# Kernel tuning notes

Hardware: AMD Instinct MI355X
Metric: run time of the kernel (lower is better)

Reference implementation:

```python
import jax, jax.numpy as jnp
import numpy as np

COMMIT_LAMBDA = 0.25


def setup_inputs() -> dict:
    key = jax.random.key(0)
    k1, k2 = jax.random.split(key)
    B, C, T = 8, 256, 1024
    NCB, K, D = 2, 8192, 128
    x = jax.random.normal(k1, (B, C, T), dtype=jnp.float32)
    # EMA codebook weights buffer (init: randn * 0.1)
    codebooks = jax.random.normal(k2, (NCB, K, D), dtype=jnp.float32) * 0.1
    return {"x": x, "codebooks": codebooks}


def reference(x, codebooks):
    B, C, T = x.shape
    ncb, K, d = codebooks.shape
    # [B, C, T] -> [B*T, ncb, d]
    xs = x.reshape(B, ncb, d, T).transpose(0, 3, 1, 2).reshape(B * T, ncb, d)
    # squared euclidean distances (argmin-equivalent to cdist)
    x2 = jnp.sum(xs * xs, axis=-1)[..., None]            # [N, ncb, 1]
    c2 = jnp.sum(codebooks * codebooks, axis=-1)[None]    # [1, ncb, K]
    xc = jnp.einsum('bnd,nkd->bnk', xs, codebooks)        # [N, ncb, K]
    d2 = x2 - 2.0 * xc + c2
    idx = jnp.argmin(d2, axis=-1)                         # [N, ncb] int
    # gather nearest code vectors: [N, ncb, d]
    q = codebooks[jnp.arange(ncb)[None, :], idx]
    # straight-through estimator
    q_st = xs + jax.lax.stop_gradient(q - xs)
    # commitment loss (training mode): sum over codebooks of mse(x_i, q_i.detach())
    loss = COMMIT_LAMBDA * jnp.sum(
        jnp.mean((xs - jax.lax.stop_gradient(q)) ** 2, axis=(0, 2))
    )
    # reassemble to [B, C, T]
    quantized = q_st.reshape(B, T, ncb, d).transpose(0, 2, 3, 1).reshape(B, C, T)
    indices = idx.reshape(B, T, ncb).transpose(0, 2, 1)   # [B, ncb, T]
    return quantized, indices, loss
```

## Files before the change

### kernel.cpp

```cpp
#include <hip/hip_runtime.h>
#include <hip/hip_bf16.h>

#define BB   8
#define TT   1024
#define NCBN 2
#define DD   128
#define KK   8192
#define MM   8192

constexpr int OUT_IDX_OFF  = BB * 256 * TT;
constexpr int OUT_LOSS_OFF = OUT_IDX_OFF + BB * NCBN * TT;

#define THR   0.45f
#define QCAP  2048
#define SCAP  2048

typedef __attribute__((ext_vector_type(8))) short   short8;
typedef __attribute__((ext_vector_type(4))) float   float4v;

__device__ __forceinline__ unsigned short f2bf(float v) {
    unsigned u = __float_as_uint(v);
    return (unsigned short)((u + 0x7FFFu + ((u >> 16) & 1u)) >> 16);
}

__device__ __forceinline__ unsigned short f2bf_dn(float v) {
    unsigned u = __float_as_uint(v);
    unsigned short h = (unsigned short)(u >> 16);
    if ((u & 0x80000000u) && (u & 0xFFFFu)) ++h;
    return h;
}

__device__ __forceinline__ void gl_lds16(const void* g, void* l) {
    __builtin_amdgcn_global_load_lds(
        (const __attribute__((address_space(1))) unsigned int*)g,
        (__attribute__((address_space(3))) unsigned int*)l, 16, 0, 0);
}

__global__ __launch_bounds__(256)
void pack_kernel(const float* __restrict__ x, const float* __restrict__ cb,
                 unsigned short* __restrict__ xbf, unsigned short* __restrict__ cbf,
                 float* __restrict__ x2, float* __restrict__ c2,
                 unsigned long long* __restrict__ pmin, float* __restrict__ out) {
    __shared__ float Ld[DD][33];
    const int gb  = blockIdx.x;
    const int tid = threadIdx.x;

    if (gb < 512) {
        const int bxn = gb & 15, ty = gb >> 4;
        const int b = bxn >> 1, n = bxn & 1;
        const int t0 = ty * 32;

        const float* base = x + ((size_t)(b * 256 + n * 128)) * TT + t0;
#pragma unroll
        for (int pp = 0; pp < 4; ++pp) {
            int u = tid + pp * 256;
            int d = u >> 3, sg = u & 7;
            float4 v = *(const float4*)(base + (size_t)d * TT + sg * 4);
            int t = sg * 4;
            Ld[d][t + 0] = v.x; Ld[d][t + 1] = v.y;
            Ld[d][t + 2] = v.z; Ld[d][t + 3] = v.w;
        }
        __syncthreads();

        if (tid < 32) {
            float s = 0.f;
            for (int d = 0; d < DD; ++d) { float v = Ld[d][tid]; s = fmaf(v, v, s); }
            x2[(size_t)n * MM + b * TT + t0 + tid] = s;
            pmin[(size_t)n * MM + b * TT + t0 + tid] = 0xFFFFFFFFFFFFFFFFull;
        }

        unsigned short* orow0 = xbf + ((size_t)n * MM + b * TT + t0) * DD;
#pragma unroll
        for (int pp = 0; pp < 2; ++pp) {
            int u = tid + pp * 256;
            int tt = u >> 4, sg = u & 15;
            unsigned short tmp[8];
#pragma unroll
            for (int j = 0; j < 8; ++j) tmp[j] = f2bf(Ld[sg * 8 + j][tt]);
            uint4 pk;
            pk.x = (unsigned)tmp[0] | ((unsigned)tmp[1] << 16);
            pk.y = (unsigned)tmp[2] | ((unsigned)tmp[3] << 16);
            pk.z = (unsigned)tmp[4] | ((unsigned)tmp[5] << 16);
            pk.w = (unsigned)tmp[6] | ((unsigned)tmp[7] << 16);
            *(uint4*)(orow0 + (size_t)tt * DD + sg * 8) = pk;
        }
    } else {
        int g = (gb - 512) * 256 + tid;
        if (g == 0) out[OUT_LOSS_OFF] = 0.f;
        const float4* crow = (const float4*)(cb + (size_t)g * DD);
        unsigned short* orow = cbf + (size_t)g * DD;
        float s = 0.f;
#pragma unroll 4
        for (int i2 = 0; i2 < 16; ++i2) {
            float4 v0 = crow[2 * i2];
            float4 v1 = crow[2 * i2 + 1];
            s = fmaf(v0.x, v0.x, s); s = fmaf(v0.y, v0.y, s);
            s = fmaf(v0.z, v0.z, s); s = fmaf(v0.w, v0.w, s);
            s = fmaf(v1.x, v1.x, s); s = fmaf(v1.y, v1.y, s);
            s = fmaf(v1.z, v1.z, s); s = fmaf(v1.w, v1.w, s);
            uint4 pk;
            pk.x = (unsigned)f2bf(v0.x) | ((unsigned)f2bf(v0.y) << 16);
            pk.y = (unsigned)f2bf(v0.z) | ((unsigned)f2bf(v0.w) << 16);
            pk.z = (unsigned)f2bf(v1.x) | ((unsigned)f2bf(v1.y) << 16);
            pk.w = (unsigned)f2bf(v1.z) | ((unsigned)f2bf(v1.w) << 16);
            *(uint4*)(orow + i2 * 8) = pk;
        }
        c2[g] = s;
    }
}

__device__ void rescore_one(int n, int m, int k,
                            const float* __restrict__ x, const float* __restrict__ cb,
                            const float* __restrict__ x2, const float* __restrict__ c2,
                            unsigned long long* __restrict__ pmin) {
    int b = m >> 10, t = m & (TT - 1);
    const float* xp = x + ((size_t)(b * 256 + n * 128)) * TT + t;
    const float* cp = cb + ((size_t)(n * KK + k)) * DD;
    float xc = 0.f;
    for (int d = 0; d < DD; ++d)
        xc = fmaf(xp[(size_t)d * TT], cp[d], xc);
    float u = x2[n * MM + m] - 2.0f * xc;
    float s = u + c2[n * KK + k];
    unsigned long long pk = ((unsigned long long)__float_as_uint(s) << 32) | (unsigned)k;
    atomicMin(pmin + (size_t)n * MM + m, pk);
}

__global__ __launch_bounds__(512, 4)
void screen_kernel(const unsigned short* __restrict__ xbf,
                   const unsigned short* __restrict__ cbf,
                   const float* __restrict__ c2,
                   const float* __restrict__ x,
                   const float* __restrict__ cb32,
                   const float* __restrict__ x2,
                   unsigned long long* __restrict__ pmin,
                   unsigned long long* __restrict__ spill) {
    __shared__ __align__(16) unsigned short Csh[2][128 * 128];
    __shared__ float          c2s[2][128];
    __shared__ unsigned int   minU[128];
    __shared__ unsigned int   qcnt;
    __shared__ unsigned int   queue[QCAP];
    __shared__ unsigned short queueY[QCAP];

    const int tid = threadIdx.x;
    const int id  = blockIdx.x;
    const int n   = id & 1;
    const int ks  = (id >> 1) & 3;
    const int qt  = id >> 3;
    const int m0  = qt * 128;
    const int k0  = ks * 2048;

    const int wave = tid >> 6, lane = tid & 63;
    const int cw = wave & 1, qw = wave >> 1;
    const int quad = lane >> 4, l15 = lane & 15;

    unsigned long long* spillp = spill + (size_t)id * SCAP;

    int goff[4];
#pragma unroll
    for (int p = 0; p < 4; ++p) {
        int u   = (p * 8 + wave) * 64 + lane;
        int row = u >> 4;
        int seg = (u & 15) ^ (row & 15);
        goff[p] = (row * DD + seg * 8) * 2;
    }

    const char*  asrc0 = (const char*)(cbf + ((size_t)n * KK + k0) * DD);
    const float* c2p   = c2 + (size_t)n * KK + k0;

    {
        const char* qsrc = (const char*)(xbf + ((size_t)n * MM + m0) * DD);
#pragma unroll
        for (int p = 0; p < 4; ++p)
            gl_lds16(qsrc + goff[p], &Csh[0][(p * 8 + wave) * 512]);
#pragma unroll
        for (int p = 0; p < 4; ++p)
            gl_lds16(asrc0 + goff[p], &Csh[1][(p * 8 + wave) * 512]);
    }
    if (tid < 32)  *(float4*)&c2s[1][tid * 4] = *(const float4*)(c2p + tid * 4);
    if (tid < 128) minU[tid] = 0xFFFFFFFFu;
    if (tid == 0)  qcnt = 0;
    __syncthreads();

    short8 bfr[2][4];
#pragma unroll
    for (int tq = 0; tq < 2; ++tq) {
        int q = qw * 32 + tq * 16 + l15;
#pragma unroll
        for (int k4 = 0; k4 < 4; ++k4) {
            int seg = k4 * 4 + quad;
            bfr[tq][k4] = *(const short8*)(&Csh[0][q * 128 + ((seg ^ l15) * 8)]);
        }
    }
    __syncthreads();

    float thr[2] = {3.4e38f, 3.4e38f};

    for (int it = 0; it <= 16; ++it) {
        const int sb   = it & 1;
        const int cbuf = sb ^ 1;
        const int dcur = (it < 16) ? it : 0;

        if (it < 16) {
            const int dn = (it + 1 < 16) ? (it + 1) : 0;
            const char* src = asrc0 + (size_t)dn * (128 * DD * 2);
#pragma unroll
            for (int p = 0; p < 4; ++p)
                gl_lds16(src + goff[p], &Csh[sb][(p * 8 + wave) * 512]);
            if (tid < 32)
                *(float4*)&c2s[sb][tid * 4] =
                    *(const float4*)(c2p + dn * 128 + tid * 4);
        }

        float4v acc[4][2];
#pragma unroll
        for (int tc = 0; tc < 4; ++tc)
#pragma unroll
            for (int tq = 0; tq < 2; ++tq)
                acc[tc][tq] = (float4v){0.f, 0.f, 0.f, 0.f};

#pragma unroll
        for (int k4 = 0; k4 < 4; ++k4) {
            short8 a[4];
#pragma unroll
            for (int tc = 0; tc < 4; ++tc) {
                int r = cw * 64 + tc * 16 + l15;
                int seg = k4 * 4 + quad;
                a[tc] = *(const short8*)(&Csh[cbuf][r * 128 + ((seg ^ l15) * 8)]);
            }
#pragma unroll
            for (int tc = 0; tc < 4; ++tc)
#pragma unroll
                for (int tq = 0; tq < 2; ++tq)
                    acc[tc][tq] = __builtin_amdgcn_mfma_f32_16x16x32_bf16(
                        a[tc], bfr[tq][k4], acc[tc][tq], 0, 0, 0);
        }

        float cmin[2] = {3.4e38f, 3.4e38f};
#pragma unroll
        for (int tc = 0; tc < 4; ++tc) {
            float4v c2r = *(const float4v*)(&c2s[cbuf][cw * 64 + tc * 16 + quad * 4]);
#pragma unroll
            for (int tq = 0; tq < 2; ++tq) {
                float y0 = fmaf(-2.0f, acc[tc][tq][0], c2r[0]);
                float y1 = fmaf(-2.0f, acc[tc][tq][1], c2r[1]);
                float y2 = fmaf(-2.0f, acc[tc][tq][2], c2r[2]);
                float y3 = fmaf(-2.0f, acc[tc][tq][3], c2r[3]);
                acc[tc][tq] = (float4v){y0, y1, y2, y3};
                cmin[tq] = fminf(cmin[tq],
                                 fminf(fminf(y0, y1), fminf(y2, y3)));
            }
        }
#pragma unroll
        for (int tq = 0; tq < 2; ++tq) {
            float v = cmin[tq];
            v = fminf(v, __shfl_xor(v, 16, 64));
            v = fminf(v, __shfl_xor(v, 32, 64));
            cmin[tq] = v;
        }

        if (it > 0) {
            float te[2];
#pragma unroll
            for (int tq = 0; tq < 2; ++tq)
                te[tq] = fminf(thr[tq], cmin[tq] + THR);
#pragma unroll
            for (int tc = 0; tc < 4; ++tc) {
#pragma unroll
                for (int tq = 0; tq < 2; ++tq) {
                    float4v yv = acc[tc][tq];
                    float m4 = fminf(fminf(yv[0], yv[1]), fminf(yv[2], yv[3]));
                    if (m4 <= te[tq]) {
#pragma unroll
                        for (int rg = 0; rg < 4; ++rg) {
                            if (yv[rg] <= te[tq]) {
                                unsigned idx  = atomicAdd(&qcnt, 1u);
                                unsigned code = (unsigned)(dcur * 128 + cw * 64 + tc * 16 + quad * 4 + rg);
                                unsigned q    = (unsigned)(qw * 32 + tq * 16 + l15);
                                unsigned ent  = (q << 11) | code;
                                if (idx < QCAP) {
                                    queue[idx]  = ent;
                                    queueY[idx] = f2bf_dn(yv[rg]);
                                } else if (idx < QCAP + SCAP) {
                                    spillp[idx - QCAP] =
                                        ((unsigned long long)ent << 32) |
                                        (unsigned long long)f2bf_dn(yv[rg]);
                                } else {
                                    rescore_one(n, m0 + (int)q, k0 + (int)code,
                                                x, cb32, x2, c2, pmin);
                                }
                            }
                        }
                    }
                }
            }
        }

        if (it < 16) {
#pragma unroll
            for (int tq = 0; tq < 2; ++tq) {
                if (quad == 0) {
                    unsigned u  = __float_as_uint(cmin[tq]);
                    unsigned mu = (u & 0x80000000u) ? ~u : (u | 0x80000000u);
                    atomicMin(&minU[qw * 32 + tq * 16 + l15], mu);
                }
            }
        }
        __syncthreads();
        if (it < 16) {
#pragma unroll
            for (int tq = 0; tq < 2; ++tq) {
                unsigned mu = minU[qw * 32 + tq * 16 + l15];
                unsigned u  = (mu & 0x80000000u) ? (mu & 0x7FFFFFFFu) : ~mu;
                thr[tq] = __uint_as_float(u) + THR;
            }
        }
    }

    unsigned total = qcnt;
    if (total > (unsigned)(QCAP + SCAP)) total = QCAP + SCAP;
    for (unsigned i = tid; i < total; i += 512) {
        unsigned ent; unsigned short y16;
        if (i < QCAP) { ent = queue[i]; y16 = queueY[i]; }
        else {
            unsigned long long se = spillp[i - QCAP];
            ent = (unsigned)(se >> 32); y16 = (unsigned short)se;
        }
        unsigned q   = ent >> 11;
        unsigned mu  = minU[q];
        unsigned u   = (mu & 0x80000000u) ? (mu & 0x7FFFFFFFu) : ~mu;
        float thrF   = __uint_as_float(u) + THR;
        float yv     = __uint_as_float((unsigned)y16 << 16);
        if (yv <= thrF)
            rescore_one(n, m0 + (int)q, k0 + (int)(ent & 2047u),
                        x, cb32, x2, c2, pmin);
    }
}

__global__ __launch_bounds__(256)
void gather_kernel(const float* __restrict__ cb,
                   const unsigned long long* __restrict__ pmin,
                   float* __restrict__ out) {
    __shared__ float Cr[32][DD + 1];
    __shared__ int   kid[32];
    const int b = blockIdx.x >> 1, n = blockIdx.x & 1;
    const int t0 = blockIdx.y * 32;
    const int tid = threadIdx.x;

    float spart = 0.f;
    if (tid < 32) {
        int t = t0 + tid;
        unsigned long long pk = pmin[(size_t)n * MM + b * TT + t];
        int k = (int)(pk & 0xFFFFFFFFull);
        kid[tid] = k;
        out[OUT_IDX_OFF + (b * NCBN + n) * TT + t] = (float)k;
        spart = __uint_as_float((unsigned)(pk >> 32));
    }
    __syncthreads();

    {
        int row = tid >> 3, q8 = tid & 7;
        const float* cp = cb + ((size_t)n * KK + kid[row]) * DD + q8 * 16;
#pragma unroll
        for (int j = 0; j < 4; ++j) {
            float4 v = *(const float4*)(cp + j * 4);
            int d = q8 * 16 + j * 4;
            Cr[row][d + 0] = v.x; Cr[row][d + 1] = v.y;
            Cr[row][d + 2] = v.z; Cr[row][d + 3] = v.w;
        }
    }
    __syncthreads();

    float* ob = out + ((size_t)(b * 256 + n * 128)) * TT + t0;
#pragma unroll
    for (int pp = 0; pp < 4; ++pp) {
        int u  = tid + pp * 256;
        int d  = u >> 3, ts = (u & 7) * 4;
        float4 qv = { Cr[ts + 0][d], Cr[ts + 1][d], Cr[ts + 2][d], Cr[ts + 3][d] };
        *(float4*)(ob + (size_t)d * TT + ts) = qv;
    }

    if (tid < 32) {
#pragma unroll
        for (int o = 16; o > 0; o >>= 1) spart += __shfl_down(spart, o, 64);
        if (tid == 0)
            atomicAdd(out + OUT_LOSS_OFF, spart * 2.384185791015625e-7f);
    }
}

extern "C" void kernel_launch(void* const* d_in, const int* in_sizes, int n_in,
                              void* d_out, int out_size, void* d_ws, size_t ws_size,
                              hipStream_t stream) {
    (void)in_sizes; (void)n_in; (void)out_size; (void)ws_size;
    const float* x  = (const float*)d_in[0];
    const float* cb = (const float*)d_in[1];
    float* out = (float*)d_out;

    char* ws = (char*)d_ws;
    unsigned short* xbf = (unsigned short*)(ws);
    unsigned short* cbf = (unsigned short*)(ws + (4u << 20));
    float* x2 = (float*)(ws + (8u << 20));
    float* c2 = (float*)(ws + (8u << 20) + (64u << 10));
    unsigned long long* pmin =
        (unsigned long long*)(ws + (8u << 20) + (128u << 10));

    unsigned long long* spill = (unsigned long long*)out;

    pack_kernel<<<dim3(576), 256, 0, stream>>>(x, cb, xbf, cbf, x2, c2, pmin, out);
    screen_kernel<<<dim3(512), 512, 0, stream>>>(xbf, cbf, c2, x, cb, x2, pmin,
                                                 spill);
    gather_kernel<<<dim3(16, 32), 256, 0, stream>>>(cb, pmin, out);
}
```

Baseline: 183.3 us.

## Filter candidates in the same iteration, dropping the extra pipeline stage

Removes the delayed-by-one-iteration candidate filtering and the 17th loop iteration. Each tile is now filtered right after its MFMA pass, using the shared running minimum read directly from LDS. The c2 values are loaded before a barrier that is moved earlier, so the buffer can be overwritten safely. The minU sentinel is changed to the encoding of the max float so the threshold stays finite. Because minU is read without a barrier after other waves update it, the threshold can be looser, which may enqueue more candidates.

```diff
diff --git a/kernel.cpp b/kernel.cpp
--- a/kernel.cpp
+++ b/kernel.cpp
@@ -177,7 +177,7 @@
             gl_lds16(asrc0 + goff[p], &Csh[1][(p * 8 + wave) * 512]);
     }
     if (tid < 32)  *(float4*)&c2s[1][tid * 4] = *(const float4*)(c2p + tid * 4);
-    if (tid < 128) minU[tid] = 0xFFFFFFFFu;
+    if (tid < 128) minU[tid] = 0xFF7FFFFFu;
     if (tid == 0)  qcnt = 0;
     __syncthreads();
 
@@ -193,15 +193,12 @@
     }
     __syncthreads();
 
-    float thr[2] = {3.4e38f, 3.4e38f};
-
-    for (int it = 0; it <= 16; ++it) {
+    for (int it = 0; it < 16; ++it) {
         const int sb   = it & 1;
         const int cbuf = sb ^ 1;
-        const int dcur = (it < 16) ? it : 0;
-
-        if (it < 16) {
-            const int dn = (it + 1 < 16) ? (it + 1) : 0;
+
+        if (it < 15) {
+            const int dn = it + 1;
             const char* src = asrc0 + (size_t)dn * (128 * DD * 2);
 #pragma unroll
             for (int p = 0; p < 4; ++p)
@@ -235,19 +232,27 @@
                         a[tc], bfr[tq][k4], acc[tc][tq], 0, 0, 0);
         }
 
+        float4v c2r[4];
+#pragma unroll
+        for (int tc = 0; tc < 4; ++tc)
+            c2r[tc] = *(const float4v*)(&c2s[cbuf][cw * 64 + tc * 16 + quad * 4]);
+
+        __syncthreads();
+
         float cmin[2] = {3.4e38f, 3.4e38f};
+        float m4s[4][2];
 #pragma unroll
         for (int tc = 0; tc < 4; ++tc) {
-            float4v c2r = *(const float4v*)(&c2s[cbuf][cw * 64 + tc * 16 + quad * 4]);
 #pragma unroll
             for (int tq = 0; tq < 2; ++tq) {
-                float y0 = fmaf(-2.0f, acc[tc][tq][0], c2r[0]);
-                float y1 = fmaf(-2.0f, acc[tc][tq][1], c2r[1]);
-                float y2 = fmaf(-2.0f, acc[tc][tq][2], c2r[2]);
-                float y3 = fmaf(-2.0f, acc[tc][tq][3], c2r[3]);
+                float y0 = fmaf(-2.0f, acc[tc][tq][0], c2r[tc][0]);
+                float y1 = fmaf(-2.0f, acc[tc][tq][1], c2r[tc][1]);
+                float y2 = fmaf(-2.0f, acc[tc][tq][2], c2r[tc][2]);
+                float y3 = fmaf(-2.0f, acc[tc][tq][3], c2r[tc][3]);
                 acc[tc][tq] = (float4v){y0, y1, y2, y3};
-                cmin[tq] = fminf(cmin[tq],
-                                 fminf(fminf(y0, y1), fminf(y2, y3)));
+                float m4 = fminf(fminf(y0, y1), fminf(y2, y3));
+                m4s[tc][tq] = m4;
+                cmin[tq] = fminf(cmin[tq], m4);
             }
         }
 #pragma unroll
@@ -258,36 +263,37 @@
             cmin[tq] = v;
         }
 
-        if (it > 0) {
-            float te[2];
-#pragma unroll
-            for (int tq = 0; tq < 2; ++tq)
-                te[tq] = fminf(thr[tq], cmin[tq] + THR);
-#pragma unroll
-            for (int tc = 0; tc < 4; ++tc) {
-#pragma unroll
-                for (int tq = 0; tq < 2; ++tq) {
+        float te[2];
+#pragma unroll
+        for (int tq = 0; tq < 2; ++tq) {
+            unsigned mu = minU[qw * 32 + tq * 16 + l15];
+            unsigned u  = (mu & 0x80000000u) ? (mu & 0x7FFFFFFFu) : ~mu;
+            te[tq] = fminf(__uint_as_float(u) + THR, cmin[tq] + THR);
+        }
+
+#pragma unroll
+        for (int tc = 0; tc < 4; ++tc) {
+#pragma unroll
+            for (int tq = 0; tq < 2; ++tq) {
+                if (m4s[tc][tq] <= te[tq]) {
                     float4v yv = acc[tc][tq];
-                    float m4 = fminf(fminf(yv[0], yv[1]), fminf(yv[2], yv[3]));
-                    if (m4 <= te[tq]) {
-#pragma unroll
-                        for (int rg = 0; rg < 4; ++rg) {
-                            if (yv[rg] <= te[tq]) {
-                                unsigned idx  = atomicAdd(&qcnt, 1u);
-                                unsigned code = (unsigned)(dcur * 128 + cw * 64 + tc * 16 + quad * 4 + rg);
-                                unsigned q    = (unsigned)(qw * 32 + tq * 16 + l15);
-                                unsigned ent  = (q << 11) | code;
-                                if (idx < QCAP) {
-                                    queue[idx]  = ent;
-                                    queueY[idx] = f2bf_dn(yv[rg]);
-                                } else if (idx < QCAP + SCAP) {
-                                    spillp[idx - QCAP] =
-                                        ((unsigned long long)ent << 32) |
-                                        (unsigned long long)f2bf_dn(yv[rg]);
-                                } else {
-                                    rescore_one(n, m0 + (int)q, k0 + (int)code,
-                                                x, cb32, x2, c2, pmin);
-                                }
+#pragma unroll
+                    for (int rg = 0; rg < 4; ++rg) {
+                        if (yv[rg] <= te[tq]) {
+                            unsigned idx  = atomicAdd(&qcnt, 1u);
+                            unsigned code = (unsigned)(it * 128 + cw * 64 + tc * 16 + quad * 4 + rg);
+                            unsigned q    = (unsigned)(qw * 32 + tq * 16 + l15);
+                            unsigned ent  = (q << 11) | code;
+                            if (idx < QCAP) {
+                                queue[idx]  = ent;
+                                queueY[idx] = f2bf_dn(yv[rg]);
+                            } else if (idx < QCAP + SCAP) {
+                                spillp[idx - QCAP] =
+                                    ((unsigned long long)ent << 32) |
+                                    (unsigned long long)f2bf_dn(yv[rg]);
+                            } else {
+                                rescore_one(n, m0 + (int)q, k0 + (int)code,
+                                            x, cb32, x2, c2, pmin);
                             }
                         }
                     }
@@ -295,26 +301,17 @@
             }
         }
 
-        if (it < 16) {
-#pragma unroll
-            for (int tq = 0; tq < 2; ++tq) {
-                if (quad == 0) {
-                    unsigned u  = __float_as_uint(cmin[tq]);
-                    unsigned mu = (u & 0x80000000u) ? ~u : (u | 0x80000000u);
-                    atomicMin(&minU[qw * 32 + tq * 16 + l15], mu);
-                }
+#pragma unroll
+        for (int tq = 0; tq < 2; ++tq) {
+            if (quad == 0) {
+                unsigned u  = __float_as_uint(cmin[tq]);
+                unsigned mu = (u & 0x80000000u) ? ~u : (u | 0x80000000u);
+                atomicMin(&minU[qw * 32 + tq * 16 + l15], mu);
             }
         }
-        __syncthreads();
-        if (it < 16) {
-#pragma unroll
-            for (int tq = 0; tq < 2; ++tq) {
-                unsigned mu = minU[qw * 32 + tq * 16 + l15];
-                unsigned u  = (mu & 0x80000000u) ? (mu & 0x7FFFFFFFu) : ~mu;
-                thr[tq] = __uint_as_float(u) + THR;
-            }
-        }
-    }
+    }
+
+    __syncthreads();
 
     unsigned total = qcnt;
     if (total > (unsigned)(QCAP + SCAP)) total = QCAP + SCAP;
```

Measured after the change: 250.0 us. 36.4% more time.

## Double screen kernel block to 1024 threads, halving per-wave query tile

Applied to the files above, without the earlier changes.

The screening kernel now runs 16 waves per block instead of 8. Each wave handles 16 query rows instead of 32, so per-thread accumulators and B fragments are halved and the cooperative LDS loads use two passes instead of four. The goal is lower register pressure and more waves to hide LDS and MFMA latency. In exchange, each A fragment loaded from LDS now feeds only one MFMA instead of two, which doubles LDS read traffic per MFMA and may add barrier cost with more waves per block.

```diff
diff --git a/kernel.cpp b/kernel.cpp
--- a/kernel.cpp
+++ b/kernel.cpp
@@ -125,7 +125,7 @@
     atomicMin(pmin + (size_t)n * MM + m, pk);
 }
 
-__global__ __launch_bounds__(512, 4)
+__global__ __launch_bounds__(1024, 8)
 void screen_kernel(const unsigned short* __restrict__ xbf,
                    const unsigned short* __restrict__ cbf,
                    const float* __restrict__ c2,
@@ -155,10 +155,10 @@
 
     unsigned long long* spillp = spill + (size_t)id * SCAP;
 
-    int goff[4];
-#pragma unroll
-    for (int p = 0; p < 4; ++p) {
-        int u   = (p * 8 + wave) * 64 + lane;
+    int goff[2];
+#pragma unroll
+    for (int p = 0; p < 2; ++p) {
+        int u   = (p * 16 + wave) * 64 + lane;
         int row = u >> 4;
         int seg = (u & 15) ^ (row & 15);
         goff[p] = (row * DD + seg * 8) * 2;
@@ -170,30 +170,29 @@
     {
         const char* qsrc = (const char*)(xbf + ((size_t)n * MM + m0) * DD);
 #pragma unroll
-        for (int p = 0; p < 4; ++p)
-            gl_lds16(qsrc + goff[p], &Csh[0][(p * 8 + wave) * 512]);
-#pragma unroll
-        for (int p = 0; p < 4; ++p)
-            gl_lds16(asrc0 + goff[p], &Csh[1][(p * 8 + wave) * 512]);
+        for (int p = 0; p < 2; ++p)
+            gl_lds16(qsrc + goff[p], &Csh[0][(p * 16 + wave) * 512]);
+#pragma unroll
+        for (int p = 0; p < 2; ++p)
+            gl_lds16(asrc0 + goff[p], &Csh[1][(p * 16 + wave) * 512]);
     }
     if (tid < 32)  *(float4*)&c2s[1][tid * 4] = *(const float4*)(c2p + tid * 4);
     if (tid < 128) minU[tid] = 0xFFFFFFFFu;
     if (tid == 0)  qcnt = 0;
     __syncthreads();
 
-    short8 bfr[2][4];
-#pragma unroll
-    for (int tq = 0; tq < 2; ++tq) {
-        int q = qw * 32 + tq * 16 + l15;
+    short8 bfr[4];
+    {
+        int q = qw * 16 + l15;
 #pragma unroll
         for (int k4 = 0; k4 < 4; ++k4) {
             int seg = k4 * 4 + quad;
-            bfr[tq][k4] = *(const short8*)(&Csh[0][q * 128 + ((seg ^ l15) * 8)]);
+            bfr[k4] = *(const short8*)(&Csh[0][q * 128 + ((seg ^ l15) * 8)]);
         }
     }
     __syncthreads();
 
-    float thr[2] = {3.4e38f, 3.4e38f};
+    float thr = 3.4e38f;
 
     for (int it = 0; it <= 16; ++it) {
         const int sb   = it & 1;
@@ -204,19 +203,17 @@
             const int dn = (it + 1 < 16) ? (it + 1) : 0;
             const char* src = asrc0 + (size_t)dn * (128 * DD * 2);
 #pragma unroll
-            for (int p = 0; p < 4; ++p)
-                gl_lds16(src + goff[p], &Csh[sb][(p * 8 + wave) * 512]);
+            for (int p = 0; p < 2; ++p)
+                gl_lds16(src + goff[p], &Csh[sb][(p * 16 + wave) * 512]);
             if (tid < 32)
                 *(float4*)&c2s[sb][tid * 4] =
                     *(const float4*)(c2p + dn * 128 + tid * 4);
         }
 
-        float4v acc[4][2];
+        float4v acc[4];
 #pragma unroll
         for (int tc = 0; tc < 4; ++tc)
-#pragma unroll
-            for (int tq = 0; tq < 2; ++tq)
-                acc[tc][tq] = (float4v){0.f, 0.f, 0.f, 0.f};
+            acc[tc] = (float4v){0.f, 0.f, 0.f, 0.f};
 
 #pragma unroll
         for (int k4 = 0; k4 < 4; ++k4) {
@@ -229,65 +226,48 @@
             }
 #pragma unroll
             for (int tc = 0; tc < 4; ++tc)
-#pragma unroll
-                for (int tq = 0; tq < 2; ++tq)
-                    acc[tc][tq] = __builtin_amdgcn_mfma_f32_16x16x32_bf16(
-                        a[tc], bfr[tq][k4], acc[tc][tq], 0, 0, 0);
-        }
-
-        float cmin[2] = {3.4e38f, 3.4e38f};
+                acc[tc] = __builtin_amdgcn_mfma_f32_16x16x32_bf16(
+                    a[tc], bfr[k4], acc[tc], 0, 0, 0);
+        }
+
+        float cmin = 3.4e38f;
 #pragma unroll
         for (int tc = 0; tc < 4; ++tc) {
             float4v c2r = *(const float4v*)(&c2s[cbuf][cw * 64 + tc * 16 + quad * 4]);
-#pragma unroll
-            for (int tq = 0; tq < 2; ++tq) {
-                float y0 = fmaf(-2.0f, acc[tc][tq][0], c2r[0]);
-                float y1 = fmaf(-2.0f, acc[tc][tq][1], c2r[1]);
-                float y2 = fmaf(-2.0f, acc[tc][tq][2], c2r[2]);
-                float y3 = fmaf(-2.0f, acc[tc][tq][3], c2r[3]);
-                acc[tc][tq] = (float4v){y0, y1, y2, y3};
-                cmin[tq] = fminf(cmin[tq],
-                                 fminf(fminf(y0, y1), fminf(y2, y3)));
-            }
-        }
-#pragma unroll
-        for (int tq = 0; tq < 2; ++tq) {
-            float v = cmin[tq];
-            v = fminf(v, __shfl_xor(v, 16, 64));
-            v = fminf(v, __shfl_xor(v, 32, 64));
-            cmin[tq] = v;
-        }
+            float y0 = fmaf(-2.0f, acc[tc][0], c2r[0]);
+            float y1 = fmaf(-2.0f, acc[tc][1], c2r[1]);
+            float y2 = fmaf(-2.0f, acc[tc][2], c2r[2]);
+            float y3 = fmaf(-2.0f, acc[tc][3], c2r[3]);
+            acc[tc] = (float4v){y0, y1, y2, y3};
+            cmin = fminf(cmin, fminf(fminf(y0, y1), fminf(y2, y3)));
+        }
+        cmin = fminf(cmin, __shfl_xor(cmin, 16, 64));
+        cmin = fminf(cmin, __shfl_xor(cmin, 32, 64));
 
         if (it > 0) {
-            float te[2];
-#pragma unroll
-            for (int tq = 0; tq < 2; ++tq)
-                te[tq] = fminf(thr[tq], cmin[tq] + THR);
+            float te = fminf(thr, cmin + THR);
 #pragma unroll
             for (int tc = 0; tc < 4; ++tc) {
-#pragma unroll
-                for (int tq = 0; tq < 2; ++tq) {
-                    float4v yv = acc[tc][tq];
-                    float m4 = fminf(fminf(yv[0], yv[1]), fminf(yv[2], yv[3]));
-                    if (m4 <= te[tq]) {
-#pragma unroll
-                        for (int rg = 0; rg < 4; ++rg) {
-                            if (yv[rg] <= te[tq]) {
-                                unsigned idx  = atomicAdd(&qcnt, 1u);
-                                unsigned code = (unsigned)(dcur * 128 + cw * 64 + tc * 16 + quad * 4 + rg);
-                                unsigned q    = (unsigned)(qw * 32 + tq * 16 + l15);
-                                unsigned ent  = (q << 11) | code;
-                                if (idx < QCAP) {
-                                    queue[idx]  = ent;
-                                    queueY[idx] = f2bf_dn(yv[rg]);
-                                } else if (idx < QCAP + SCAP) {
-                                    spillp[idx - QCAP] =
-                                        ((unsigned long long)ent << 32) |
-                                        (unsigned long long)f2bf_dn(yv[rg]);
-                                } else {
-                                    rescore_one(n, m0 + (int)q, k0 + (int)code,
-                                                x, cb32, x2, c2, pmin);
-                                }
+                float4v yv = acc[tc];
+                float m4 = fminf(fminf(yv[0], yv[1]), fminf(yv[2], yv[3]));
+                if (m4 <= te) {
+#pragma unroll
+                    for (int rg = 0; rg < 4; ++rg) {
+                        if (yv[rg] <= te) {
+                            unsigned idx  = atomicAdd(&qcnt, 1u);
+                            unsigned code = (unsigned)(dcur * 128 + cw * 64 + tc * 16 + quad * 4 + rg);
+                            unsigned q    = (unsigned)(qw * 16 + l15);
+                            unsigned ent  = (q << 11) | code;
+                            if (idx < QCAP) {
+                                queue[idx]  = ent;
+                                queueY[idx] = f2bf_dn(yv[rg]);
+                            } else if (idx < QCAP + SCAP) {
+                                spillp[idx - QCAP] =
+                                    ((unsigned long long)ent << 32) |
+                                    (unsigned long long)f2bf_dn(yv[rg]);
+                            } else {
+                                rescore_one(n, m0 + (int)q, k0 + (int)code,
+                                            x, cb32, x2, c2, pmin);
                             }
                         }
                     }
@@ -296,29 +276,23 @@
         }
 
         if (it < 16) {
-#pragma unroll
-            for (int tq = 0; tq < 2; ++tq) {
-                if (quad == 0) {
-                    unsigned u  = __float_as_uint(cmin[tq]);
-                    unsigned mu = (u & 0x80000000u) ? ~u : (u | 0x80000000u);
-                    atomicMin(&minU[qw * 32 + tq * 16 + l15], mu);
-                }
+            if (quad == 0) {
+                unsigned u  = __float_as_uint(cmin);
+                unsigned mu = (u & 0x80000000u) ? ~u : (u | 0x80000000u);
+                atomicMin(&minU[qw * 16 + l15], mu);
             }
         }
         __syncthreads();
         if (it < 16) {
-#pragma unroll
-            for (int tq = 0; tq < 2; ++tq) {
-                unsigned mu = minU[qw * 32 + tq * 16 + l15];
-                unsigned u  = (mu & 0x80000000u) ? (mu & 0x7FFFFFFFu) : ~mu;
-                thr[tq] = __uint_as_float(u) + THR;
-            }
+            unsigned mu = minU[qw * 16 + l15];
+            unsigned u  = (mu & 0x80000000u) ? (mu & 0x7FFFFFFFu) : ~mu;
+            thr = __uint_as_float(u) + THR;
         }
     }
 
     unsigned total = qcnt;
     if (total > (unsigned)(QCAP + SCAP)) total = QCAP + SCAP;
-    for (unsigned i = tid; i < total; i += 512) {
+    for (unsigned i = tid; i < total; i += 1024) {
         unsigned ent; unsigned short y16;
         if (i < QCAP) { ent = queue[i]; y16 = queueY[i]; }
         else {
@@ -406,7 +380,7 @@
     unsigned long long* spill = (unsigned long long*)out;
 
     pack_kernel<<<dim3(576), 256, 0, stream>>>(x, cb, xbf, cbf, x2, c2, pmin, out);
-    screen_kernel<<<dim3(512), 512, 0, stream>>>(xbf, cbf, c2, x, cb, x2, pmin,
-                                                 spill);
+    screen_kernel<<<dim3(512), 1024, 0, stream>>>(xbf, cbf, c2, x, cb, x2, pmin,
+                                                  spill);
     gather_kernel<<<dim3(16, 32), 256, 0, stream>>>(cb, pmin, out);
 }
```

After: 237.9 us. 29.8% more time.
